# Kernel optimization log

Measured on AMD Instinct MI355X. Metric: run time of the kernel, lower is better.

Reference implementation:

```python
import jax, jax.numpy as jnp
import numpy as np

B, H, W, N = 8, 384, 384, 96
STEPSZ = 0.1; ALPHA = 0.01; BETA = 0.01; STD = 1.0
NSTEPS = 50; NSTEPS_W = 10; DMAX = 15.0; EXTGRADFAC = 10.0

def make_gauss_edge_fltr(std):
    # Gaussian-derivative edge filters, one per spatial dim: [2,1,k,k]
    r = int(np.ceil(3 * std)); t = np.arange(-r, r + 1, dtype=np.float32)
    g = np.exp(-t * t / (2 * std * std)); g /= g.sum()
    dg = -t / (std * std) * np.exp(-t * t / (2 * std * std)); dg /= np.abs(dg).sum()
    fy = np.outer(dg, g)   # d/drow
    fx = np.outer(g, dg)   # d/dcol
    return np.stack([fy, fx])[:, None].astype(np.float32)

def setup_inputs() -> dict:
    key = jax.random.key(0)
    k1, k2 = jax.random.split(key, 2)
    pred_dmap = jax.random.normal(k1, (B, 1, H, W), jnp.float32)
    nodes = jax.random.uniform(k2, (B, N, 2), jnp.float32)
    nodes = nodes * jnp.array([H - 1.0, W - 1.0], jnp.float32)
    nodes = jnp.sort(nodes, axis=1)  # roughly monotone chain -> path-like snake
    widths = jnp.ones((B, N), jnp.float32) * 3.0
    fltr = jnp.asarray(make_gauss_edge_fltr(STD))
    return {"pred_dmap": pred_dmap, "nodes": nodes, "widths": widths, "fltr": fltr}

def grad_im(x, fltr):
    # x: [B,1,H,W], fltr: [2,1,k,k] -> [B,2,H,W]
    return jax.lax.conv_general_dilated(x, fltr, (1, 1), 'SAME',
                                        dimension_numbers=('NCHW', 'OIHW', 'NCHW'))

def interp(img, pts):
    # bilinear sample: img [C,H,W], pts [N,2] (row,col) -> [N,C]
    C, Hh, Ww = img.shape
    y = jnp.clip(pts[:, 0], 0.0, Hh - 1.0); x = jnp.clip(pts[:, 1], 0.0, Ww - 1.0)
    y0 = jnp.floor(y).astype(jnp.int32); x0 = jnp.floor(x).astype(jnp.int32)
    y1 = jnp.minimum(y0 + 1, Hh - 1); x1 = jnp.minimum(x0 + 1, Ww - 1)
    wy = y - y0; wx = x - x0
    v00 = img[:, y0, x0]; v01 = img[:, y0, x1]
    v10 = img[:, y1, x0]; v11 = img[:, y1, x1]
    v = v00 * (1 - wy) * (1 - wx) + v01 * (1 - wy) * wx + v10 * wy * (1 - wx) + v11 * wy * wx
    return v.T

def d2_open(x):
    # second difference with replicated endpoints (open snake)
    xp = jnp.concatenate([x[:1], x, x[-1:]], 0)
    return xp[:-2] - 2 * xp[1:-1] + xp[2:]

def snake_one(nodes, widths, g, gw):
    # explicit active-contour iterations on node positions
    def pstep(x, _):
        fext = interp(g, x)                       # [N,2] external force
        d2 = d2_open(x); d4 = d2_open(d2)
        return x + STEPSZ * (ALPHA * d2 - BETA * d4 + fext), None
    x, _ = jax.lax.scan(pstep, nodes, None, length=NSTEPS)
    # unit normals from central-difference tangents
    t = jnp.concatenate([x[1:2] - x[0:1], 0.5 * (x[2:] - x[:-2]), x[-1:] - x[-2:-1]], 0)
    n = jnp.stack([-t[:, 1], t[:, 0]], 1)
    n = n / (jnp.linalg.norm(n, axis=1, keepdims=True) + 1e-6)
    def wstep(w, _):
        gp = interp(gw, x + w[:, None] * n); gm = interp(gw, x - w[:, None] * n)
        f = 0.5 * (jnp.sum(gp * n, 1) - jnp.sum(gm * n, 1))
        return jnp.maximum(w + STEPSZ * f, 0.5), None
    w, _ = jax.lax.scan(wstep, widths, None, length=NSTEPS_W)
    return x, w

def render(x, w):
    # distance-to-ribbon map, clipped at DMAX; only [HW,S] intermediates
    ys, xs = jnp.meshgrid(jnp.arange(H, dtype=jnp.float32),
                          jnp.arange(W, dtype=jnp.float32), indexing='ij')
    P = jnp.stack([ys.ravel(), xs.ravel()], 1)          # [HW,2]
    a = x[:-1]; ab = x[1:] - a                          # [S,2]
    denom = jnp.sum(ab * ab, 1) + 1e-8                  # [S]
    dotpa = P @ ab.T - jnp.sum(a * ab, 1)               # [HW,S] = (P-a).ab
    t = jnp.clip(dotpa / denom, 0.0, 1.0)
    pa2 = jnp.sum(P * P, 1)[:, None] - 2 * (P @ a.T) + jnp.sum(a * a, 1)  # |P-a|^2
    d = jnp.sqrt(jnp.maximum(pa2 - 2 * t * dotpa + t * t * denom, 0.0))
    ws = 0.5 * (w[:-1] + w[1:])                         # per-segment width
    dmap = jnp.min(jnp.maximum(d - ws, 0.0), axis=1)
    return jnp.minimum(dmap, DMAX).reshape(H, W)

def reference(pred_dmap, nodes, widths, fltr):
    gimg = grad_im(pred_dmap, fltr) * EXTGRADFAC          # [B,2,H,W]
    gimgW = grad_im(jnp.abs(pred_dmap), fltr) * EXTGRADFAC
    def per_sample(nd, wd, g, gw):
        x, w = snake_one(nd, wd, g, gw)
        return render(x, w)
    dm = jax.vmap(per_sample)(nodes, widths, gimg, gimgW)[:, None]  # [B,1,H,W]
    dm = jax.lax.stop_gradient(dm)   # snake_dm.detach() in the original
    return jnp.mean((pred_dmap - dm) ** 2)
```

## Files before the change

### kernel.cpp

```cpp
#include <hip/hip_runtime.h>
#include <math.h>

#define BB   8
#define HH   384
#define WW   384
#define NN   96
#define HWSZ (HH * WW)
#define NSEG (NN - 1)
#define SEGF 12
#define SEGPAD 1152
#define DMAXV 15.0f
#define ROWS_PER_BLK 12
#define NCHUNK (HH / ROWS_PER_BLK)
#define CROWS 12
#define CBANDS (HH / CROWS)
#define MAGICU 0x9E3779B9u

typedef unsigned long long u64;
typedef unsigned int u32;

__device__ inline void st_pair(float* p, float lo, float hi)
{
    u64 v = ((u64)__float_as_uint(hi) << 32) | (u64)__float_as_uint(lo);
    __hip_atomic_store((u64*)p, v, __ATOMIC_RELAXED, __HIP_MEMORY_SCOPE_AGENT);
}

__device__ inline float ld_f32_coh(const float* p)
{
    u32 v = __hip_atomic_load((u32*)p, __ATOMIC_RELAXED, __HIP_MEMORY_SCOPE_AGENT);
    return __uint_as_float(v);
}

#define WAIT_ALL() asm volatile("s_waitcnt vmcnt(0) lgkmcnt(0)" ::: "memory")

__device__ inline void load_taps(const float* __restrict__ fltr,
                                 float* __restrict__ sg, float* __restrict__ sdg)
{
    int tid = threadIdx.x;
    if (tid < 7) {
        float s = 0.f;
#pragma unroll
        for (int i = 0; i < 7; ++i) s += fabsf(fltr[i * 7 + tid]);
        sg[tid] = s;
    } else if (tid < 14) {
        int r = tid - 7;
        float s = 0.f;
#pragma unroll
        for (int j = 0; j < 7; ++j) s += fltr[r * 7 + j];
        sdg[r] = s;
    }
    __syncthreads();
}

__global__ __launch_bounds__(384) void conv_fused(
    const float* __restrict__ pred, const float* __restrict__ fltr,
    float2* __restrict__ g2, float2* __restrict__ gw2)
{
    __shared__ float sg[7], sdg[7];
    load_taps(fltr, sg, sdg);

    int blk = blockIdx.x;
    int b = blk & 7;
    int band = blk >> 3;
    int y0 = band * CROWS;
    int x = threadIdx.x;
    const float* pb = pred + (size_t)b * HWSZ;
    bool xin = (x >= 3) && (x < WW - 3);

    float hg[7], hd[7], hga[7], hda[7];

#pragma unroll
    for (int q = 0; q < CROWS + 6; ++q) {
        float vg = 0.f, vd = 0.f, vga = 0.f, vda = 0.f;
        int r = y0 + q - 3;
        if (r >= 0 && r < HH) {
            const float* row = pb + r * WW;
            if (xin) {
#pragma unroll
                for (int k = 0; k < 7; ++k) {
                    float v  = row[x + k - 3];
                    float av = fabsf(v);
                    vg  = fmaf(v,  sg[k],  vg);
                    vd  = fmaf(v,  sdg[k], vd);
                    vga = fmaf(av, sg[k],  vga);
                    vda = fmaf(av, sdg[k], vda);
                }
            } else {
#pragma unroll
                for (int k = 0; k < 7; ++k) {
                    int ix = x + k - 3;
                    float v  = (ix >= 0 && ix < WW) ? row[ix] : 0.f;
                    float av = fabsf(v);
                    vg  = fmaf(v,  sg[k],  vg);
                    vd  = fmaf(v,  sdg[k], vd);
                    vga = fmaf(av, sg[k],  vga);
                    vda = fmaf(av, sdg[k], vda);
                }
            }
        }
        hg[q % 7] = vg; hd[q % 7] = vd; hga[q % 7] = vga; hda[q % 7] = vda;

        if (q >= 6) {
            int y = y0 + q - 6;
            float o0 = 0.f, o1 = 0.f, o2 = 0.f, o3 = 0.f;
#pragma unroll
            for (int j = 0; j < 7; ++j) {
                int s = (q - 6 + j) % 7;
                o0 = fmaf(hg[s],  sdg[j], o0);
                o1 = fmaf(hd[s],  sg[j],  o1);
                o2 = fmaf(hga[s], sdg[j], o2);
                o3 = fmaf(hda[s], sg[j],  o3);
            }
            size_t gi = (size_t)b * HWSZ + (size_t)y * WW + x;
            g2[gi]  = make_float2(o0 * 10.f, o1 * 10.f);
            gw2[gi] = make_float2(o2 * 10.f, o3 * 10.f);
        }
    }
}

__device__ inline float2 bilin2i(const float2* __restrict__ img, float py, float px)
{
    float y = fminf(fmaxf(py, 0.0f), (float)(HH - 1));
    float x = fminf(fmaxf(px, 0.0f), (float)(WW - 1));
    int y0 = (int)floorf(y);
    int x0 = (int)floorf(x);
    int y1 = min(y0 + 1, HH - 1);
    bool xedge = (x0 + 1 > WW - 1);
    float wy = y - (float)y0;
    float wx = x - (float)x0;
    float4 r0 = *(const float4*)(img + y0 * WW + x0);
    float4 r1 = *(const float4*)(img + y1 * WW + x0);
    float2 v00 = make_float2(r0.x, r0.y);
    float2 v01 = xedge ? v00 : make_float2(r0.z, r0.w);
    float2 v10 = make_float2(r1.x, r1.y);
    float2 v11 = xedge ? v10 : make_float2(r1.z, r1.w);
    float w00 = (1.f - wy) * (1.f - wx);
    float w01 = (1.f - wy) * wx;
    float w10 = wy * (1.f - wx);
    float w11 = wy * wx;
    return make_float2(v00.x * w00 + v01.x * w01 + v10.x * w10 + v11.x * w11,
                       v00.y * w00 + v01.y * w01 + v10.y * w10 + v11.y * w11);
}

__device__ inline void write_seg_wt(float* __restrict__ r,
                                    float py, float px, float qy, float qx, float wseg)
{
    float aby = qy - py, abx = qx - px;
    float denom = aby * aby + abx * abx + 1e-8f;
    float aab = py * aby + px * abx;
    float aa  = py * py + px * px;
    float reach = DMAXV + wseg;
    st_pair(r + 0,  py,  px);
    st_pair(r + 2,  aby, abx);
    st_pair(r + 4,  aab, denom);
    st_pair(r + 6,  1.0f / denom, aa);
    st_pair(r + 8,  wseg, fminf(py, qy) - reach);
    st_pair(r + 10, fmaxf(py, qy) + reach, 0.f);
}

__global__ __launch_bounds__(384) void snake_render(
    const float* __restrict__ pred, const float* __restrict__ nodes,
    const float* __restrict__ widths,
    const float* __restrict__ g2f, const float* __restrict__ gw2f,
    float* __restrict__ segs, u64* __restrict__ pflag,
    u32* __restrict__ segflag, float* __restrict__ out)
{
    __shared__ float ss[NSEG * SEGF];
    __shared__ float2 posb[2][NN];
    __shared__ float  wbuf[NN];
    __shared__ int slo, shi;
    __shared__ float swsum[6];

    int blk = blockIdx.x;
    int b   = blk & 7;
    int band = blk >> 3;
    int t = threadIdx.x;

    int y0r = band * ROWS_PER_BLK;
    const float* pb = pred + (size_t)b * HWSZ + (size_t)y0r * WW + t;
    float pv[ROWS_PER_BLK];
#pragma unroll
    for (int ry = 0; ry < ROWS_PER_BLK; ++ry) pv[ry] = pb[ry * WW];

    if (t == 0) { slo = NSEG; shi = -1; }

    if (blk < 8) {
        const float2* gb  = (const float2*)g2f  + (size_t)b * HWSZ;
        const float2* gwb = (const float2*)gw2f + (size_t)b * HWSZ;
        int wv = t >> 6, ln = t & 63;
        int n  = wv * 48 + ln;
        bool act = (wv < 2) && (ln < 48);
        bool n0f = (n == 0), nlf = (n == NN - 1);

        float py = 0.f, px = 0.f;
        if (act) {
            float2 p0 = *(const float2*)(nodes + (size_t)(b * NN + n) * 2);
            py = p0.x; px = p0.y;
            posb[0][n] = p0;
        }
        __syncthreads();

        for (int s = 0; s < 50; ++s) {
            const float2* pcur = posb[s & 1];
            float2* pnxt = posb[(s & 1) ^ 1];
            if (act) {
                float yc = fminf(fmaxf(py, 0.0f), (float)(HH - 1));
                float xc = fminf(fmaxf(px, 0.0f), (float)(WW - 1));
                int y0i = (int)floorf(yc);
                int x0i = (int)floorf(xc);
                int y1i = min(y0i + 1, HH - 1);
                bool xedge = (x0i + 1 > WW - 1);
                float wy = yc - (float)y0i;
                float wx = xc - (float)x0i;
                float4 r0 = *(const float4*)(gb + y0i * WW + x0i);
                float4 r1 = *(const float4*)(gb + y1i * WW + x0i);

                float2 xm1 = pcur[max(n - 1, 0)];
                float2 xp1 = pcur[min(n + 1, NN - 1)];
                float2 xm2 = pcur[max(n - 2, 0)];
                float2 xp2 = pcur[min(n + 2, NN - 1)];

                float d2m_y = xm2.x - 2.f * xm1.x + py;
                float d2c_y = xm1.x - 2.f * py + xp1.x;
                float d2p_y = py - 2.f * xp1.x + xp2.x;
                float d2m_x = xm2.y - 2.f * xm1.y + px;
                float d2c_x = xm1.y - 2.f * px + xp1.y;
                float d2p_x = px - 2.f * xp1.y + xp2.y;
                d2m_y = n0f ? d2c_y : d2m_y;
                d2m_x = n0f ? d2c_x : d2m_x;
                d2p_y = nlf ? d2c_y : d2p_y;
                d2p_x = nlf ? d2c_x : d2p_x;
                float d4_y = d2m_y - 2.f * d2c_y + d2p_y;
                float d4_x = d2m_x - 2.f * d2c_x + d2p_x;

                float2 v00 = make_float2(r0.x, r0.y);
                float2 v01 = xedge ? v00 : make_float2(r0.z, r0.w);
                float2 v10 = make_float2(r1.x, r1.y);
                float2 v11 = xedge ? v10 : make_float2(r1.z, r1.w);
                float w00 = (1.f - wy) * (1.f - wx);
                float w01 = (1.f - wy) * wx;
                float w10 = wy * (1.f - wx);
                float w11 = wy * wx;
                float fy = v00.x * w00 + v01.x * w01 + v10.x * w10 + v11.x * w11;
                float fx = v00.y * w00 + v01.y * w01 + v10.y * w10 + v11.y * w11;

                py += 0.1f * (0.01f * d2c_y - 0.01f * d4_y + fy);
                px += 0.1f * (0.01f * d2c_x - 0.01f * d4_x + fx);
                pnxt[n] = make_float2(py, px);
            }
            __syncthreads();
        }

        float ny_ = 0.f, nx_ = 0.f, wn = 0.f;
        if (act) {
            float2 xm1 = posb[0][max(n - 1, 0)];
            float2 xp1 = posb[0][min(n + 1, NN - 1)];
            float ty, tx;
            if (n0f)      { ty = xp1.x - py;  tx = xp1.y - px; }
            else if (nlf) { ty = py - xm1.x;  tx = px - xm1.y; }
            else          { ty = 0.5f * (xp1.x - xm1.x); tx = 0.5f * (xp1.y - xm1.y); }

            float nn0 = -tx, nn1 = ty;
            float nrm = sqrtf(nn0 * nn0 + nn1 * nn1) + 1e-6f;
            ny_ = nn0 / nrm; nx_ = nn1 / nrm;

            wn = widths[b * NN + n];
            for (int s = 0; s < 10; ++s) {
                float2 gp = bilin2i(gwb, py + wn * ny_, px + wn * nx_);
                float2 gm = bilin2i(gwb, py - wn * ny_, px - wn * nx_);
                float fw = 0.5f * ((gp.x * ny_ + gp.y * nx_) - (gm.x * ny_ + gm.y * nx_));
                wn = fmaxf(wn + 0.1f * fw, 0.5f);
            }
            wbuf[n] = wn;
        }
        __syncthreads();

        if (act && n < NSEG) {
            float2 q = posb[0][n + 1];
            float wq = wbuf[n + 1];
            write_seg_wt(segs + (size_t)b * SEGPAD + (size_t)n * SEGF,
                         py, px, q.x, q.y, 0.5f * (wn + wq));
        }
        WAIT_ALL();
        __syncthreads();
        if (t == 0)
            __hip_atomic_store(&segflag[b], MAGICU,
                               __ATOMIC_RELAXED, __HIP_MEMORY_SCOPE_AGENT);
    } else {
        if (t == 0) {
            while (__hip_atomic_load(&segflag[b],
                                     __ATOMIC_RELAXED, __HIP_MEMORY_SCOPE_AGENT) != MAGICU)
                __builtin_amdgcn_s_sleep(8);
            asm volatile("" ::: "memory");
        }
    }

    __syncthreads();

    {
        int y0 = y0r;
        const float* sb = segs + (size_t)b * SEGPAD;
        for (int j = t; j < NSEG * SEGF; j += 384)
            ss[j] = ld_f32_coh(sb + j);
        __syncthreads();

        float cy0 = (float)y0, cy1 = (float)(y0 + ROWS_PER_BLK - 1);
        if (t < NSEG) {
            float ylo = ss[t * SEGF + 9];
            float yhi = ss[t * SEGF + 10];
            if (yhi >= cy0 && ylo <= cy1) {
                atomicMin(&slo, t);
                atomicMax(&shi, t);
            }
        }
        __syncthreads();
        int lo = slo, hi = shi;

        float px = (float)t;
        float px2 = px * px;
        float minv[ROWS_PER_BLK];
#pragma unroll
        for (int r = 0; r < ROWS_PER_BLK; ++r) minv[r] = DMAXV;

        for (int si = lo; si <= hi; ++si) {
            const float* r = ss + si * SEGF;
            float ax = r[1], abx = r[3], ws = r[8];
            float bxe = ax + abx;
            float reach = DMAXV + ws + 0.01f;
            if (px < fminf(ax, bxe) - reach || px > fmaxf(ax, bxe) + reach) continue;

            float ay = r[0], aby = r[2];
            float aab = r[4], denom = r[5], invd = r[6], aa = r[7];
            float dotpa_b = fmaf(px, abx, -aab);
            float pa2_b   = fmaf(px, -2.0f * ax, px2 + aa);
#pragma unroll
            for (int ry = 0; ry < ROWS_PER_BLK; ++ry) {
                float py = (float)(y0 + ry);
                float dotpa = fmaf(py, aby, dotpa_b);
                float tt = fminf(fmaxf(dotpa * invd, 0.0f), 1.0f);
                float pa2 = fmaf(py, fmaf(py, 1.0f, -2.0f * ay), pa2_b);
                float d2 = fmaf(tt, fmaf(tt, denom, -2.0f * dotpa), pa2);
                float d = sqrtf(fmaxf(d2, 0.0f));
                float v = fmaxf(d - ws, 0.0f);
                minv[ry] = fminf(minv[ry], v);
            }
        }

        float sq = 0.f;
#pragma unroll
        for (int ry = 0; ry < ROWS_PER_BLK; ++ry) {
            float diff = pv[ry] - minv[ry];
            sq = fmaf(diff, diff, sq);
        }

#pragma unroll
        for (int off = 32; off > 0; off >>= 1) sq += __shfl_down(sq, off, 64);
        if ((t & 63) == 0) swsum[t >> 6] = sq;
        __syncthreads();
        if (t == 0) {
            float tot = swsum[0] + swsum[1] + swsum[2] + swsum[3] + swsum[4] + swsum[5];
            u64 pvv = ((u64)MAGICU << 32) | (u64)__float_as_uint(tot);
            __hip_atomic_store(&pflag[blk], pvv,
                               __ATOMIC_RELAXED, __HIP_MEMORY_SCOPE_AGENT);
        }
    }

    if (blk == 8) {
        __syncthreads();
        float v = 0.f;
        if (t < 256) {
            u64 pvv = __hip_atomic_load(&pflag[t], __ATOMIC_RELAXED,
                                        __HIP_MEMORY_SCOPE_AGENT);
            while ((u32)(pvv >> 32) != MAGICU) {
                __builtin_amdgcn_s_sleep(4);
                pvv = __hip_atomic_load(&pflag[t], __ATOMIC_RELAXED,
                                        __HIP_MEMORY_SCOPE_AGENT);
            }
            v = __uint_as_float((u32)pvv);
        }
#pragma unroll
        for (int off = 32; off > 0; off >>= 1) v += __shfl_down(v, off, 64);
        if ((t & 63) == 0) swsum[t >> 6] = v;
        __syncthreads();
        if (t == 0) {
            float tot = swsum[0] + swsum[1] + swsum[2] + swsum[3] + swsum[4] + swsum[5];
            out[0] = tot * (1.0f / (float)(BB * HWSZ));
        }
    }
}

extern "C" void kernel_launch(void* const* d_in, const int* in_sizes, int n_in,
                              void* d_out, int out_size, void* d_ws, size_t ws_size,
                              hipStream_t stream)
{
    const float* pred   = (const float*)d_in[0];
    const float* nodes  = (const float*)d_in[1];
    const float* widths = (const float*)d_in[2];
    const float* fltr   = (const float*)d_in[3];
    float* out = (float*)d_out;

    float* ws   = (float*)d_ws;
    float* g2   = ws;
    float* gw2  = g2 + (size_t)2 * BB * HWSZ;
    float* segs = gw2 + (size_t)2 * BB * HWSZ;
    float* tail = segs + (size_t)BB * SEGPAD + 256;
    u64* pflag = (u64*)tail;
    u32* segflag = (u32*)(pflag + 256);

    conv_fused<<<BB * CBANDS, 384, 0, stream>>>(pred, fltr,
                                                (float2*)g2, (float2*)gw2);
    snake_render<<<BB * NCHUNK, 384, 0, stream>>>(pred, nodes, widths, g2, gw2,
                                                  segs, pflag, segflag, out);
}
```

Baseline: 121.3 us.

## Split snake and render into separate kernels, prefetch gradients a step ahead

Replaces the single fused snake+render kernel, whose render blocks spin-waited on a per-sample flag, with a 128-thread snake kernel followed by a separate render kernel launched after it on the same stream. The snake loop now issues the bilinear gradient loads for the next step before the barrier so global latency overlaps the LDS stencil, and it uses a lighter LDS-only barrier. Atomic coherent stores and loads for segments are replaced by plain stores. This trades in-kernel spin waiting for an extra kernel launch boundary, and render blocks can no longer load pred while the snake runs.

Result: no change. 119.6 us (-1.4%).

```diff
diff --git a/kernel.cpp b/kernel.cpp
--- a/kernel.cpp
+++ b/kernel.cpp
@@ -18,20 +18,6 @@
 
 typedef unsigned long long u64;
 typedef unsigned int u32;
-
-__device__ inline void st_pair(float* p, float lo, float hi)
-{
-    u64 v = ((u64)__float_as_uint(hi) << 32) | (u64)__float_as_uint(lo);
-    __hip_atomic_store((u64*)p, v, __ATOMIC_RELAXED, __HIP_MEMORY_SCOPE_AGENT);
-}
-
-__device__ inline float ld_f32_coh(const float* p)
-{
-    u32 v = __hip_atomic_load((u32*)p, __ATOMIC_RELAXED, __HIP_MEMORY_SCOPE_AGENT);
-    return __uint_as_float(v);
-}
-
-#define WAIT_ALL() asm volatile("s_waitcnt vmcnt(0) lgkmcnt(0)" ::: "memory")
 
 __device__ inline void load_taps(const float* __restrict__ fltr,
                                  float* __restrict__ sg, float* __restrict__ sdg)
@@ -142,227 +128,238 @@
                        v00.y * w00 + v01.y * w01 + v10.y * w10 + v11.y * w11);
 }
 
-__device__ inline void write_seg_wt(float* __restrict__ r,
-                                    float py, float px, float qy, float qx, float wseg)
+__device__ inline void write_seg(float* __restrict__ r,
+                                 float py, float px, float qy, float qx, float wseg)
 {
     float aby = qy - py, abx = qx - px;
     float denom = aby * aby + abx * abx + 1e-8f;
     float aab = py * aby + px * abx;
     float aa  = py * py + px * px;
     float reach = DMAXV + wseg;
-    st_pair(r + 0,  py,  px);
-    st_pair(r + 2,  aby, abx);
-    st_pair(r + 4,  aab, denom);
-    st_pair(r + 6,  1.0f / denom, aa);
-    st_pair(r + 8,  wseg, fminf(py, qy) - reach);
-    st_pair(r + 10, fmaxf(py, qy) + reach, 0.f);
-}
-
-__global__ __launch_bounds__(384) void snake_render(
-    const float* __restrict__ pred, const float* __restrict__ nodes,
-    const float* __restrict__ widths,
+    r[0]  = py;   r[1]  = px;
+    r[2]  = aby;  r[3]  = abx;
+    r[4]  = aab;  r[5]  = denom;
+    r[6]  = 1.0f / denom;
+    r[7]  = aa;   r[8]  = wseg;
+    r[9]  = fminf(py, qy) - reach;
+    r[10] = fmaxf(py, qy) + reach;
+    r[11] = 0.f;
+}
+
+__device__ inline void lds_barrier()
+{
+    asm volatile("s_waitcnt lgkmcnt(0)" ::: "memory");
+    __builtin_amdgcn_sched_barrier(0);
+    __builtin_amdgcn_s_barrier();
+    __builtin_amdgcn_sched_barrier(0);
+}
+
+__global__ __launch_bounds__(128) void snake_kernel(
+    const float* __restrict__ nodes, const float* __restrict__ widths,
     const float* __restrict__ g2f, const float* __restrict__ gw2f,
-    float* __restrict__ segs, u64* __restrict__ pflag,
-    u32* __restrict__ segflag, float* __restrict__ out)
-{
-    __shared__ float ss[NSEG * SEGF];
+    float* __restrict__ segs)
+{
     __shared__ float2 posb[2][NN];
     __shared__ float  wbuf[NN];
+
+    int b = blockIdx.x;
+    int t = threadIdx.x;
+    int wv = t >> 6, ln = t & 63;
+    int n  = wv * 48 + ln;
+    bool act = (ln < 48);
+    bool n0f = (n == 0), nlf = (n == NN - 1);
+
+    const float2* gb  = (const float2*)g2f  + (size_t)b * HWSZ;
+    const float2* gwb = (const float2*)gw2f + (size_t)b * HWSZ;
+
+    float py = 0.f, px = 0.f;
+    float4 r0 = make_float4(0.f, 0.f, 0.f, 0.f), r1 = r0;
+    float wy = 0.f, wx = 0.f;
+    bool xedge = false;
+
+    if (act) {
+        float2 p0 = *(const float2*)(nodes + (size_t)(b * NN + n) * 2);
+        py = p0.x; px = p0.y;
+        posb[0][n] = p0;
+        float yc = fminf(fmaxf(py, 0.0f), (float)(HH - 1));
+        float xc = fminf(fmaxf(px, 0.0f), (float)(WW - 1));
+        int y0i = (int)floorf(yc);
+        int x0i = (int)floorf(xc);
+        int y1i = min(y0i + 1, HH - 1);
+        xedge = (x0i + 1 > WW - 1);
+        wy = yc - (float)y0i;
+        wx = xc - (float)x0i;
+        r0 = *(const float4*)(gb + y0i * WW + x0i);
+        r1 = *(const float4*)(gb + y1i * WW + x0i);
+    }
+    lds_barrier();
+
+    for (int s = 0; s < 50; ++s) {
+        const float2* pcur = posb[s & 1];
+        float2* pnxt = posb[(s & 1) ^ 1];
+        if (act) {
+            float2 xm1 = pcur[max(n - 1, 0)];
+            float2 xp1 = pcur[min(n + 1, NN - 1)];
+            float2 xm2 = pcur[max(n - 2, 0)];
+            float2 xp2 = pcur[min(n + 2, NN - 1)];
+
+            float d2m_y = xm2.x - 2.f * xm1.x + py;
+            float d2c_y = xm1.x - 2.f * py + xp1.x;
+            float d2p_y = py - 2.f * xp1.x + xp2.x;
+            float d2m_x = xm2.y - 2.f * xm1.y + px;
+            float d2c_x = xm1.y - 2.f * px + xp1.y;
+            float d2p_x = px - 2.f * xp1.y + xp2.y;
+            d2m_y = n0f ? d2c_y : d2m_y;
+            d2m_x = n0f ? d2c_x : d2m_x;
+            d2p_y = nlf ? d2c_y : d2p_y;
+            d2p_x = nlf ? d2c_x : d2p_x;
+            float d4_y = d2m_y - 2.f * d2c_y + d2p_y;
+            float d4_x = d2m_x - 2.f * d2c_x + d2p_x;
+
+            float2 v00 = make_float2(r0.x, r0.y);
+            float2 v01 = xedge ? v00 : make_float2(r0.z, r0.w);
+            float2 v10 = make_float2(r1.x, r1.y);
+            float2 v11 = xedge ? v10 : make_float2(r1.z, r1.w);
+            float w00 = (1.f - wy) * (1.f - wx);
+            float w01 = (1.f - wy) * wx;
+            float w10 = wy * (1.f - wx);
+            float w11 = wy * wx;
+            float fy = v00.x * w00 + v01.x * w01 + v10.x * w10 + v11.x * w11;
+            float fx = v00.y * w00 + v01.y * w01 + v10.y * w10 + v11.y * w11;
+
+            py += 0.1f * (0.01f * d2c_y - 0.01f * d4_y + fy);
+            px += 0.1f * (0.01f * d2c_x - 0.01f * d4_x + fx);
+
+            float yc = fminf(fmaxf(py, 0.0f), (float)(HH - 1));
+            float xc = fminf(fmaxf(px, 0.0f), (float)(WW - 1));
+            int y0i = (int)floorf(yc);
+            int x0i = (int)floorf(xc);
+            int y1i = min(y0i + 1, HH - 1);
+            xedge = (x0i + 1 > WW - 1);
+            wy = yc - (float)y0i;
+            wx = xc - (float)x0i;
+            r0 = *(const float4*)(gb + y0i * WW + x0i);
+            r1 = *(const float4*)(gb + y1i * WW + x0i);
+
+            pnxt[n] = make_float2(py, px);
+        }
+        lds_barrier();
+    }
+
+    float ny_ = 0.f, nx_ = 0.f, wn = 0.f;
+    if (act) {
+        float2 xm1 = posb[0][max(n - 1, 0)];
+        float2 xp1 = posb[0][min(n + 1, NN - 1)];
+        float ty, tx;
+        if (n0f)      { ty = xp1.x - py;  tx = xp1.y - px; }
+        else if (nlf) { ty = py - xm1.x;  tx = px - xm1.y; }
+        else          { ty = 0.5f * (xp1.x - xm1.x); tx = 0.5f * (xp1.y - xm1.y); }
+
+        float nn0 = -tx, nn1 = ty;
+        float nrm = sqrtf(nn0 * nn0 + nn1 * nn1) + 1e-6f;
+        ny_ = nn0 / nrm; nx_ = nn1 / nrm;
+
+        wn = widths[b * NN + n];
+        for (int s = 0; s < 10; ++s) {
+            float2 gp = bilin2i(gwb, py + wn * ny_, px + wn * nx_);
+            float2 gm = bilin2i(gwb, py - wn * ny_, px - wn * nx_);
+            float fw = 0.5f * ((gp.x * ny_ + gp.y * nx_) - (gm.x * ny_ + gm.y * nx_));
+            wn = fmaxf(wn + 0.1f * fw, 0.5f);
+        }
+        wbuf[n] = wn;
+    }
+    __syncthreads();
+
+    if (act && n < NSEG) {
+        float2 q = posb[0][n + 1];
+        float wq = wbuf[n + 1];
+        write_seg(segs + (size_t)b * SEGPAD + (size_t)n * SEGF,
+                  py, px, q.x, q.y, 0.5f * (wn + wq));
+    }
+}
+
+__global__ __launch_bounds__(384) void render_kernel(
+    const float* __restrict__ pred, const float* __restrict__ segs,
+    u64* __restrict__ pflag, float* __restrict__ out)
+{
+    __shared__ float ss[NSEG * SEGF];
     __shared__ int slo, shi;
     __shared__ float swsum[6];
 
     int blk = blockIdx.x;
-    int b   = blk & 7;
+    int b = blk & 7;
     int band = blk >> 3;
+    int y0 = band * ROWS_PER_BLK;
     int t = threadIdx.x;
 
-    int y0r = band * ROWS_PER_BLK;
-    const float* pb = pred + (size_t)b * HWSZ + (size_t)y0r * WW + t;
+    const float* pb = pred + (size_t)b * HWSZ + (size_t)y0 * WW + t;
     float pv[ROWS_PER_BLK];
 #pragma unroll
     for (int ry = 0; ry < ROWS_PER_BLK; ++ry) pv[ry] = pb[ry * WW];
 
+    const float* sb = segs + (size_t)b * SEGPAD;
+    for (int j = t; j < NSEG * SEGF; j += 384) ss[j] = sb[j];
     if (t == 0) { slo = NSEG; shi = -1; }
-
-    if (blk < 8) {
-        const float2* gb  = (const float2*)g2f  + (size_t)b * HWSZ;
-        const float2* gwb = (const float2*)gw2f + (size_t)b * HWSZ;
-        int wv = t >> 6, ln = t & 63;
-        int n  = wv * 48 + ln;
-        bool act = (wv < 2) && (ln < 48);
-        bool n0f = (n == 0), nlf = (n == NN - 1);
-
-        float py = 0.f, px = 0.f;
-        if (act) {
-            float2 p0 = *(const float2*)(nodes + (size_t)(b * NN + n) * 2);
-            py = p0.x; px = p0.y;
-            posb[0][n] = p0;
-        }
-        __syncthreads();
-
-        for (int s = 0; s < 50; ++s) {
-            const float2* pcur = posb[s & 1];
-            float2* pnxt = posb[(s & 1) ^ 1];
-            if (act) {
-                float yc = fminf(fmaxf(py, 0.0f), (float)(HH - 1));
-                float xc = fminf(fmaxf(px, 0.0f), (float)(WW - 1));
-                int y0i = (int)floorf(yc);
-                int x0i = (int)floorf(xc);
-                int y1i = min(y0i + 1, HH - 1);
-                bool xedge = (x0i + 1 > WW - 1);
-                float wy = yc - (float)y0i;
-                float wx = xc - (float)x0i;
-                float4 r0 = *(const float4*)(gb + y0i * WW + x0i);
-                float4 r1 = *(const float4*)(gb + y1i * WW + x0i);
-
-                float2 xm1 = pcur[max(n - 1, 0)];
-                float2 xp1 = pcur[min(n + 1, NN - 1)];
-                float2 xm2 = pcur[max(n - 2, 0)];
-                float2 xp2 = pcur[min(n + 2, NN - 1)];
-
-                float d2m_y = xm2.x - 2.f * xm1.x + py;
-                float d2c_y = xm1.x - 2.f * py + xp1.x;
-                float d2p_y = py - 2.f * xp1.x + xp2.x;
-                float d2m_x = xm2.y - 2.f * xm1.y + px;
-                float d2c_x = xm1.y - 2.f * px + xp1.y;
-                float d2p_x = px - 2.f * xp1.y + xp2.y;
-                d2m_y = n0f ? d2c_y : d2m_y;
-                d2m_x = n0f ? d2c_x : d2m_x;
-                d2p_y = nlf ? d2c_y : d2p_y;
-                d2p_x = nlf ? d2c_x : d2p_x;
-                float d4_y = d2m_y - 2.f * d2c_y + d2p_y;
-                float d4_x = d2m_x - 2.f * d2c_x + d2p_x;
-
-                float2 v00 = make_float2(r0.x, r0.y);
-                float2 v01 = xedge ? v00 : make_float2(r0.z, r0.w);
-                float2 v10 = make_float2(r1.x, r1.y);
-                float2 v11 = xedge ? v10 : make_float2(r1.z, r1.w);
-                float w00 = (1.f - wy) * (1.f - wx);
-                float w01 = (1.f - wy) * wx;
-                float w10 = wy * (1.f - wx);
-                float w11 = wy * wx;
-                float fy = v00.x * w00 + v01.x * w01 + v10.x * w10 + v11.x * w11;
-                float fx = v00.y * w00 + v01.y * w01 + v10.y * w10 + v11.y * w11;
-
-                py += 0.1f * (0.01f * d2c_y - 0.01f * d4_y + fy);
-                px += 0.1f * (0.01f * d2c_x - 0.01f * d4_x + fx);
-                pnxt[n] = make_float2(py, px);
-            }
-            __syncthreads();
-        }
-
-        float ny_ = 0.f, nx_ = 0.f, wn = 0.f;
-        if (act) {
-            float2 xm1 = posb[0][max(n - 1, 0)];
-            float2 xp1 = posb[0][min(n + 1, NN - 1)];
-            float ty, tx;
-            if (n0f)      { ty = xp1.x - py;  tx = xp1.y - px; }
-            else if (nlf) { ty = py - xm1.x;  tx = px - xm1.y; }
-            else          { ty = 0.5f * (xp1.x - xm1.x); tx = 0.5f * (xp1.y - xm1.y); }
-
-            float nn0 = -tx, nn1 = ty;
-            float nrm = sqrtf(nn0 * nn0 + nn1 * nn1) + 1e-6f;
-            ny_ = nn0 / nrm; nx_ = nn1 / nrm;
-
-            wn = widths[b * NN + n];
-            for (int s = 0; s < 10; ++s) {
-                float2 gp = bilin2i(gwb, py + wn * ny_, px + wn * nx_);
-                float2 gm = bilin2i(gwb, py - wn * ny_, px - wn * nx_);
-                float fw = 0.5f * ((gp.x * ny_ + gp.y * nx_) - (gm.x * ny_ + gm.y * nx_));
-                wn = fmaxf(wn + 0.1f * fw, 0.5f);
-            }
-            wbuf[n] = wn;
-        }
-        __syncthreads();
-
-        if (act && n < NSEG) {
-            float2 q = posb[0][n + 1];
-            float wq = wbuf[n + 1];
-            write_seg_wt(segs + (size_t)b * SEGPAD + (size_t)n * SEGF,
-                         py, px, q.x, q.y, 0.5f * (wn + wq));
-        }
-        WAIT_ALL();
-        __syncthreads();
-        if (t == 0)
-            __hip_atomic_store(&segflag[b], MAGICU,
-                               __ATOMIC_RELAXED, __HIP_MEMORY_SCOPE_AGENT);
-    } else {
-        if (t == 0) {
-            while (__hip_atomic_load(&segflag[b],
-                                     __ATOMIC_RELAXED, __HIP_MEMORY_SCOPE_AGENT) != MAGICU)
-                __builtin_amdgcn_s_sleep(8);
-            asm volatile("" ::: "memory");
-        }
-    }
-
     __syncthreads();
 
-    {
-        int y0 = y0r;
-        const float* sb = segs + (size_t)b * SEGPAD;
-        for (int j = t; j < NSEG * SEGF; j += 384)
-            ss[j] = ld_f32_coh(sb + j);
-        __syncthreads();
-
-        float cy0 = (float)y0, cy1 = (float)(y0 + ROWS_PER_BLK - 1);
-        if (t < NSEG) {
-            float ylo = ss[t * SEGF + 9];
-            float yhi = ss[t * SEGF + 10];
-            if (yhi >= cy0 && ylo <= cy1) {
-                atomicMin(&slo, t);
-                atomicMax(&shi, t);
-            }
-        }
-        __syncthreads();
-        int lo = slo, hi = shi;
-
-        float px = (float)t;
-        float px2 = px * px;
-        float minv[ROWS_PER_BLK];
-#pragma unroll
-        for (int r = 0; r < ROWS_PER_BLK; ++r) minv[r] = DMAXV;
-
-        for (int si = lo; si <= hi; ++si) {
-            const float* r = ss + si * SEGF;
-            float ax = r[1], abx = r[3], ws = r[8];
-            float bxe = ax + abx;
-            float reach = DMAXV + ws + 0.01f;
-            if (px < fminf(ax, bxe) - reach || px > fmaxf(ax, bxe) + reach) continue;
-
-            float ay = r[0], aby = r[2];
-            float aab = r[4], denom = r[5], invd = r[6], aa = r[7];
-            float dotpa_b = fmaf(px, abx, -aab);
-            float pa2_b   = fmaf(px, -2.0f * ax, px2 + aa);
-#pragma unroll
-            for (int ry = 0; ry < ROWS_PER_BLK; ++ry) {
-                float py = (float)(y0 + ry);
-                float dotpa = fmaf(py, aby, dotpa_b);
-                float tt = fminf(fmaxf(dotpa * invd, 0.0f), 1.0f);
-                float pa2 = fmaf(py, fmaf(py, 1.0f, -2.0f * ay), pa2_b);
-                float d2 = fmaf(tt, fmaf(tt, denom, -2.0f * dotpa), pa2);
-                float d = sqrtf(fmaxf(d2, 0.0f));
-                float v = fmaxf(d - ws, 0.0f);
-                minv[ry] = fminf(minv[ry], v);
-            }
-        }
-
-        float sq = 0.f;
+    float cy0 = (float)y0, cy1 = (float)(y0 + ROWS_PER_BLK - 1);
+    if (t < NSEG) {
+        float ylo = ss[t * SEGF + 9];
+        float yhi = ss[t * SEGF + 10];
+        if (yhi >= cy0 && ylo <= cy1) {
+            atomicMin(&slo, t);
+            atomicMax(&shi, t);
+        }
+    }
+    __syncthreads();
+    int lo = slo, hi = shi;
+
+    float px = (float)t;
+    float px2 = px * px;
+    float minv[ROWS_PER_BLK];
+#pragma unroll
+    for (int r = 0; r < ROWS_PER_BLK; ++r) minv[r] = DMAXV;
+
+    for (int si = lo; si <= hi; ++si) {
+        const float* r = ss + si * SEGF;
+        float ax = r[1], abx = r[3], ws = r[8];
+        float bxe = ax + abx;
+        float reach = DMAXV + ws + 0.01f;
+        if (px < fminf(ax, bxe) - reach || px > fmaxf(ax, bxe) + reach) continue;
+
+        float ay = r[0], aby = r[2];
+        float aab = r[4], denom = r[5], invd = r[6], aa = r[7];
+        float dotpa_b = fmaf(px, abx, -aab);
+        float pa2_b   = fmaf(px, -2.0f * ax, px2 + aa);
 #pragma unroll
         for (int ry = 0; ry < ROWS_PER_BLK; ++ry) {
-            float diff = pv[ry] - minv[ry];
-            sq = fmaf(diff, diff, sq);
-        }
-
-#pragma unroll
-        for (int off = 32; off > 0; off >>= 1) sq += __shfl_down(sq, off, 64);
-        if ((t & 63) == 0) swsum[t >> 6] = sq;
-        __syncthreads();
-        if (t == 0) {
-            float tot = swsum[0] + swsum[1] + swsum[2] + swsum[3] + swsum[4] + swsum[5];
-            u64 pvv = ((u64)MAGICU << 32) | (u64)__float_as_uint(tot);
-            __hip_atomic_store(&pflag[blk], pvv,
-                               __ATOMIC_RELAXED, __HIP_MEMORY_SCOPE_AGENT);
-        }
+            float py = (float)(y0 + ry);
+            float dotpa = fmaf(py, aby, dotpa_b);
+            float tt = fminf(fmaxf(dotpa * invd, 0.0f), 1.0f);
+            float pa2 = fmaf(py, fmaf(py, 1.0f, -2.0f * ay), pa2_b);
+            float d2 = fmaf(tt, fmaf(tt, denom, -2.0f * dotpa), pa2);
+            float d = sqrtf(fmaxf(d2, 0.0f));
+            float v = fmaxf(d - ws, 0.0f);
+            minv[ry] = fminf(minv[ry], v);
+        }
+    }
+
+    float sq = 0.f;
+#pragma unroll
+    for (int ry = 0; ry < ROWS_PER_BLK; ++ry) {
+        float diff = pv[ry] - minv[ry];
+        sq = fmaf(diff, diff, sq);
+    }
+
+#pragma unroll
+    for (int off = 32; off > 0; off >>= 1) sq += __shfl_down(sq, off, 64);
+    if ((t & 63) == 0) swsum[t >> 6] = sq;
+    __syncthreads();
+    if (t == 0) {
+        float tot = swsum[0] + swsum[1] + swsum[2] + swsum[3] + swsum[4] + swsum[5];
+        u64 pvv = ((u64)MAGICU << 32) | (u64)__float_as_uint(tot);
+        __hip_atomic_store(&pflag[blk], pvv,
+                           __ATOMIC_RELAXED, __HIP_MEMORY_SCOPE_AGENT);
     }
 
     if (blk == 8) {
@@ -405,10 +402,9 @@
     float* segs = gw2 + (size_t)2 * BB * HWSZ;
     float* tail = segs + (size_t)BB * SEGPAD + 256;
     u64* pflag = (u64*)tail;
-    u32* segflag = (u32*)(pflag + 256);
 
     conv_fused<<<BB * CBANDS, 384, 0, stream>>>(pred, fltr,
                                                 (float2*)g2, (float2*)gw2);
-    snake_render<<<BB * NCHUNK, 384, 0, stream>>>(pred, nodes, widths, g2, gw2,
-                                                  segs, pflag, segflag, out);
-}
+    snake_kernel<<<BB, 128, 0, stream>>>(nodes, widths, g2, gw2, segs);
+    render_kernel<<<BB * NCHUNK, 384, 0, stream>>>(pred, segs, pflag, out);
+}
```
